# Optimization experiments

Measured on AMD Instinct MI355X. Metric: run time of the kernel, lower is better.

## Reference

```python
import jax, jax.numpy as jnp
import numpy as np

B = 4096
P_HID = 1024
H_HID = 512
MAX_P = 128
MAX_HE = MAX_P // 3  # 42
TAU = 1.0
EPS = 1e-20


def setup_inputs() -> dict:
    key = jax.random.key(0)
    ks = jax.random.split(key, 12)
    s_p = 1.0 / np.sqrt(P_HID)
    s_h = 1.0 / np.sqrt(H_HID)
    # gumbel noise: g = -log(-log(U))
    u_p = jax.random.uniform(ks[3], (B, MAX_P, 2), minval=EPS, maxval=1.0)
    u_h = jax.random.uniform(ks[4], (B, MAX_HE, 2), minval=EPS, maxval=1.0)
    return {
        "particle_h": jax.random.normal(ks[0], (B, P_HID), jnp.float32),
        "edge_h": jax.random.normal(ks[1], (B, H_HID), jnp.float32),
        "hyperedge_h": jax.random.normal(ks[2], (B, H_HID), jnp.float32),
        "g_p": -jnp.log(-jnp.log(u_p)),
        "g_h": -jnp.log(-jnp.log(u_h)),
        "W1_p": jax.random.normal(ks[5], (P_HID, P_HID), jnp.float32) * s_p,
        "b1_p": jnp.zeros((P_HID,), jnp.float32),
        "W2_p": jax.random.normal(ks[6], (P_HID, MAX_P), jnp.float32) * s_p,
        "b2_p": jnp.zeros((MAX_P,), jnp.float32),
        "W1_h": jax.random.normal(ks[7], (H_HID, H_HID), jnp.float32) * s_h,
        "b1_h": jnp.zeros((H_HID,), jnp.float32),
        "W2_h": jax.random.normal(ks[8], (H_HID, MAX_HE), jnp.float32) * s_h,
        "b2_h": jnp.zeros((MAX_HE,), jnp.float32),
    }


def _gumbel_hard_st(logits, g, tau):
    """F.gumbel_softmax(stack([l,-l],-1), tau, hard=True)[...,0] (straight-through)."""
    y = jax.nn.softmax((jnp.stack([logits, -logits], axis=-1) + g) / tau, axis=-1)
    y0 = y[..., 0]
    hard0 = (y0 > y[..., 1]).astype(y0.dtype)
    return hard0 + y0 - jax.lax.stop_gradient(y0)


def _mlp(x, W1, b1, W2, b2):
    return jax.nn.gelu(x @ W1 + b1, approximate=False) @ W2 + b2


def reference(particle_h, edge_h, hyperedge_h, g_p, g_h,
              W1_p, b1_p, W2_p, b2_p, W1_h, b1_h, W2_h, b2_h):
    particle_logits = _mlp(particle_h, W1_p, b1_p, W2_p, b2_p)      # [B, MAX_P]
    particle_mask = _gumbel_hard_st(particle_logits, g_p, TAU)      # [B, MAX_P]
    n_particles = particle_mask.sum(axis=-1).astype(jnp.int32)      # [B]

    # Ragged edge lists as a fixed padded buffer: all C(MAX_P,2) lexicographic
    # pairs (same order as torch.combinations); pair (i,j), i<j, is valid for
    # batch b iff j < n_particles[b].
    ii, jj = jnp.triu_indices(MAX_P, k=1)
    edge_index = jnp.stack([ii, jj]).astype(jnp.int32)              # [2, E_max]
    edge_valid = jj[None, :] < n_particles[:, None]                 # [B, E_max] bool

    hyperedge_logits = _mlp(hyperedge_h, W1_h, b1_h, W2_h, b2_h)    # [B, MAX_HE]
    hyperedge_mask = _gumbel_hard_st(hyperedge_logits, g_h, TAU)
    n_hyperedges = hyperedge_mask.sum(axis=-1).astype(jnp.int32)

    return (particle_mask, n_particles, edge_index, edge_valid,
            hyperedge_mask, n_hyperedges)
```

## Files before the change

### kernel.cpp

```cpp
#include <hip/hip_runtime.h>
#include <hip/hip_bf16.h>
#include <math.h>

typedef __bf16 bf16_t;
typedef bf16_t bf16x8 __attribute__((ext_vector_type(8)));
typedef bf16_t bf16x4 __attribute__((ext_vector_type(4)));
typedef float f32x4 __attribute__((ext_vector_type(4)));
typedef unsigned int u32;

#define B_SZ 4096
#define P_HID 1024
#define H_HID 512
#define MAX_P 128
#define MAX_HE 42
#define HE_PAD 128
#define E_MAX 8128
#define E_MAX4 2032

__device__ __forceinline__ void async_cp16(const bf16_t* g, bf16_t* l) {
    __builtin_amdgcn_global_load_lds(
        (const __attribute__((address_space(1))) u32*)g,
        (__attribute__((address_space(3))) u32*)l, 16, 0, 0);
}

__device__ __forceinline__ float gelu_exact(float v) {
    return 0.5f * v * (1.f + erff(v * 0.70710678118654752f));
}

struct GemmP {
    const bf16_t *Ahi, *Alo, *BThi, *BTlo;
    const float* bias;
    bf16_t *Chi, *Clo;
    const float* g;
    float *out_mask, *out_n;
    int *ws_n;
    int N, K, NV, nx;
};

template<int MODE>
__global__ __launch_bounds__(256, 4) void gemm_pack(GemmP P, GemmP H, int pBlocks)
{
    constexpr int BM = 64, BN = 128;
    constexpr int MT = 2, NT = 4;
    constexpr int OPS_A = BM / 16;
    constexpr int OPS_B = BN / 16;
    constexpr int NOPS = 2 * OPS_A + 2 * OPS_B;

    __shared__ __align__(16) bf16_t smem[(2 * BM + 2 * BN) * 32];
    __shared__ float cnt[BM][2];
    bf16_t* const As0 = smem;
    bf16_t* const As1 = smem + BM * 32;
    bf16_t* const Bs0 = smem + 2 * BM * 32;
    bf16_t* const Bs1 = smem + 2 * BM * 32 + BN * 32;

    const bool isP = (int)blockIdx.x < pBlocks;
    const GemmP& a = isP ? P : H;
    const int bid  = isP ? blockIdx.x : blockIdx.x - pBlocks;
    const int bn   = (bid % a.nx) * BN;
    const int bm   = (bid / a.nx) * BM;
    const int K    = a.K;

    const int tid  = threadIdx.x;
    const int lane = tid & 63;
    const int wid  = tid >> 6;
    const int wm   = wid & 1;
    const int wn   = wid >> 1;

    const int srow = lane >> 2;
    const int scol = (lane & 3) * 8;
    const int fr   = lane & 15;
    const int fq   = lane >> 4;

    f32x4 acc[MT][NT];
#pragma unroll
    for (int i = 0; i < MT; ++i)
#pragma unroll
        for (int j = 0; j < NT; ++j)
            acc[i][j] = (f32x4){0.f, 0.f, 0.f, 0.f};

    const bf16_t* const gA0 = a.Ahi  + (size_t)bm * K;
    const bf16_t* const gA1 = a.Alo  + (size_t)bm * K;
    const bf16_t* const gB0 = a.BThi + (size_t)bn * K;
    const bf16_t* const gB1 = a.BTlo + (size_t)bn * K;

    for (int kt = 0; kt < K; kt += 32) {
        __syncthreads();
#pragma unroll
        for (int o = 0; o < NOPS; ++o) {
            if ((o & 3) != wid) continue;
            const bf16_t* gsrc;
            bf16_t* lbase;
            int q;
            if (o < OPS_A)                  { q = o;                     gsrc = gA0; lbase = As0; }
            else if (o < 2 * OPS_A)         { q = o - OPS_A;             gsrc = gA1; lbase = As1; }
            else if (o < 2 * OPS_A + OPS_B) { q = o - 2 * OPS_A;         gsrc = gB0; lbase = Bs0; }
            else                            { q = o - 2 * OPS_A - OPS_B; gsrc = gB1; lbase = Bs1; }
            async_cp16(gsrc + (size_t)(q * 16 + srow) * K + kt + scol,
                       lbase + q * 16 * 32);
        }
        __syncthreads();

        bf16x8 ah[MT], al[MT], bh[NT], bl[NT];
#pragma unroll
        for (int i = 0; i < MT; ++i) {
            const int row = wm * 32 + i * 16 + fr;
            ah[i] = *(const bf16x8*)(As0 + row * 32 + fq * 8);
            al[i] = *(const bf16x8*)(As1 + row * 32 + fq * 8);
        }
#pragma unroll
        for (int j = 0; j < NT; ++j) {
            const int row = wn * 64 + j * 16 + fr;
            bh[j] = *(const bf16x8*)(Bs0 + row * 32 + fq * 8);
            bl[j] = *(const bf16x8*)(Bs1 + row * 32 + fq * 8);
        }
#pragma unroll
        for (int i = 0; i < MT; ++i)
#pragma unroll
            for (int j = 0; j < NT; ++j) {
                acc[i][j] = __builtin_amdgcn_mfma_f32_16x16x32_bf16(ah[i], bh[j], acc[i][j], 0, 0, 0);
                acc[i][j] = __builtin_amdgcn_mfma_f32_16x16x32_bf16(ah[i], bl[j], acc[i][j], 0, 0, 0);
                acc[i][j] = __builtin_amdgcn_mfma_f32_16x16x32_bf16(al[i], bh[j], acc[i][j], 0, 0, 0);
            }
    }

    if (MODE == 0) {
#pragma unroll
        for (int i = 0; i < MT; ++i)
#pragma unroll
            for (int j = 0; j < NT; ++j) {
                const int col  = bn + wn * 64 + j * 16 + fr;
                const int row0 = bm + wm * 32 + i * 16 + fq * 4;
                const float bj = a.bias[col];
#pragma unroll
                for (int r = 0; r < 4; ++r) {
                    float v = gelu_exact(acc[i][j][r] + bj);
                    bf16_t h = (bf16_t)v;
                    bf16_t l = (bf16_t)(v - (float)h);
                    const size_t off = (size_t)(row0 + r) * a.N + col;
                    a.Chi[off] = h;
                    a.Clo[off] = l;
                }
            }
    } else {
        const int NV = a.NV;
#pragma unroll
        for (int i = 0; i < MT; ++i) {
#pragma unroll
            for (int r = 0; r < 4; ++r) {
                const int row_l = wm * 32 + i * 16 + fq * 4 + r;
                const int grow  = bm + row_l;
                float s = 0.f;
#pragma unroll
                for (int j = 0; j < NT; ++j) {
                    const int col = wn * 64 + j * 16 + fr;
                    if (col < NV) {
                        const float v = acc[i][j][r] + a.bias[col];
                        const size_t idx = (size_t)grow * NV + col;
                        const float g0 = a.g[2 * idx + 0];
                        const float g1 = a.g[2 * idx + 1];
                        const float m = ((v + g0) > (g1 - v)) ? 1.f : 0.f;
                        a.out_mask[idx] = m;
                        s += m;
                    }
                }
                s += __shfl_xor(s, 1, 64);
                s += __shfl_xor(s, 2, 64);
                s += __shfl_xor(s, 4, 64);
                s += __shfl_xor(s, 8, 64);
                if (fr == 0) cnt[row_l][wn] = s;
            }
        }
        __syncthreads();
        if (tid < BM) {
            const float c = cnt[tid][0] + cnt[tid][1];
            a.out_n[bm + tid] = c;
            if (a.ws_n) a.ws_n[bm + tid] = (int)c;
        }
    }
}

struct PrepArgs {
    const float *ph, *hh, *W1p, *W2p, *W1h, *W2h;
    bf16_t *pA_hi, *pA_lo, *hA_hi, *hA_lo;
    bf16_t *W1pT_hi, *W1pT_lo, *W2pT_hi, *W2pT_lo;
    bf16_t *W1hT_hi, *W1hT_lo, *W2hT_hi, *W2hT_lo;
    float *out_ei; int *ws_jj;
};

__device__ __forceinline__ void split4(const float* x, bf16_t* hi, bf16_t* lo, int i) {
    float4 v = ((const float4*)x)[i];
    float vv[4] = {v.x, v.y, v.z, v.w};
    bf16x4 h, l;
#pragma unroll
    for (int r = 0; r < 4; ++r) {
        bf16_t hh = (bf16_t)vv[r];
        h[r] = hh;
        l[r] = (bf16_t)(vv[r] - (float)hh);
    }
    ((bf16x4*)hi)[i] = h;
    ((bf16x4*)lo)[i] = l;
}

__device__ __forceinline__ void tsplit(
    const float* W, bf16_t* Thi, bf16_t* Tlo, int K, int N,
    int t, int nx, float (*sh)[33], int tid)
{
    const int n0 = (t % nx) * 32, k0 = (t / nx) * 32;
    const int tx = tid & 31, ty = tid >> 5;
    for (int r = ty; r < 32; r += 8) {
        const int n = n0 + tx;
        sh[r][tx] = (n < N) ? W[(size_t)(k0 + r) * N + n] : 0.f;
    }
    __syncthreads();
    for (int r = ty; r < 32; r += 8) {
        const float x = sh[tx][r];
        bf16_t h = (bf16_t)x;
        bf16_t l = (bf16_t)(x - (float)h);
        const size_t off = (size_t)(n0 + r) * K + k0 + tx;
        Thi[off] = h;
        Tlo[off] = l;
    }
}

__device__ __forceinline__ int tri_off(int i) { return (i * (255 - i)) >> 1; }

__global__ __launch_bounds__(256) void prep_all(PrepArgs a)
{
    __shared__ float sh[32][33];
    const int bid = blockIdx.x;
    const int tid = threadIdx.x;

    if (bid < 4096) {
        split4(a.ph, a.pA_hi, a.pA_lo, bid * 256 + tid);
    } else if (bid < 6144) {
        split4(a.hh, a.hA_hi, a.hA_lo, (bid - 4096) * 256 + tid);
    } else if (bid < 7168) {
        tsplit(a.W1p, a.W1pT_hi, a.W1pT_lo, P_HID, P_HID, bid - 6144, 32, sh, tid);
    } else if (bid < 7296) {
        tsplit(a.W2p, a.W2pT_hi, a.W2pT_lo, P_HID, MAX_P, bid - 7168, 4, sh, tid);
    } else if (bid < 7552) {
        tsplit(a.W1h, a.W1hT_hi, a.W1hT_lo, H_HID, H_HID, bid - 7296, 16, sh, tid);
    } else if (bid < 7616) {
        tsplit(a.W2h, a.W2hT_hi, a.W2hT_lo, H_HID, MAX_HE, bid - 7552, 4, sh, tid);
    } else {
        const int e = (bid - 7616) * 256 + tid;
        if (e < E_MAX) {
            int i = (int)((255.0 - sqrt(65025.0 - 8.0 * (double)e)) * 0.5);
            if (i < 0) i = 0;
            if (i > 126) i = 126;
            while (i > 0 && tri_off(i) > e) --i;
            while (i < 126 && tri_off(i + 1) <= e) ++i;
            const int j = i + 1 + (e - tri_off(i));
            a.out_ei[e] = (float)i;
            a.out_ei[E_MAX + e] = (float)j;
            a.ws_jj[e] = j;
        }
    }
}

__global__ __launch_bounds__(256) void edge_valid_kernel(
    const int* __restrict__ ws_jj, const int* __restrict__ ws_n,
    float* __restrict__ out)
{
    const int b   = blockIdx.x >> 1;
    const int seg = blockIdx.x & 1;
    const int n   = ws_n[b];
    const int base = seg * (E_MAX4 / 2);
    float* const orow = out + (size_t)b * E_MAX;
#pragma unroll
    for (int it = 0; it < 4; ++it) {
        const int q = base + it * 256 + threadIdx.x;
        if (q < base + E_MAX4 / 2) {
            const int4 j4 = ((const int4*)ws_jj)[q];
            float4 v;
            v.x = (j4.x < n) ? 1.f : 0.f;
            v.y = (j4.y < n) ? 1.f : 0.f;
            v.z = (j4.z < n) ? 1.f : 0.f;
            v.w = (j4.w < n) ? 1.f : 0.f;
            ((float4*)orow)[q] = v;
        }
    }
}

extern "C" void kernel_launch(void* const* d_in, const int* in_sizes, int n_in,
                              void* d_out, int out_size, void* d_ws, size_t ws_size,
                              hipStream_t stream)
{
    const float* particle_h  = (const float*)d_in[0];
    const float* hyperedge_h = (const float*)d_in[2];
    const float* g_p  = (const float*)d_in[3];
    const float* g_h  = (const float*)d_in[4];
    const float* W1_p = (const float*)d_in[5];
    const float* b1_p = (const float*)d_in[6];
    const float* W2_p = (const float*)d_in[7];
    const float* b2_p = (const float*)d_in[8];
    const float* W1_h = (const float*)d_in[9];
    const float* b1_h = (const float*)d_in[10];
    const float* W2_h = (const float*)d_in[11];
    const float* b2_h = (const float*)d_in[12];

    float* out = (float*)d_out;
    float* out_pmask = out;
    float* out_np    = out_pmask + (size_t)B_SZ * MAX_P;
    float* out_ei    = out_np + B_SZ;
    float* out_ev    = out_ei + 2 * E_MAX;
    float* out_hmask = out_ev + (size_t)B_SZ * E_MAX;
    float* out_nh    = out_hmask + (size_t)B_SZ * MAX_HE;

    char* w = (char*)d_ws;
    bf16_t* pA_hi   = (bf16_t*)w;  w += (size_t)B_SZ * P_HID * 2;
    bf16_t* pA_lo   = (bf16_t*)w;  w += (size_t)B_SZ * P_HID * 2;
    bf16_t* hA_hi   = (bf16_t*)w;  w += (size_t)B_SZ * H_HID * 2;
    bf16_t* hA_lo   = (bf16_t*)w;  w += (size_t)B_SZ * H_HID * 2;
    bf16_t* hidp_hi = (bf16_t*)w;  w += (size_t)B_SZ * P_HID * 2;
    bf16_t* hidp_lo = (bf16_t*)w;  w += (size_t)B_SZ * P_HID * 2;
    bf16_t* hidh_hi = (bf16_t*)w;  w += (size_t)B_SZ * H_HID * 2;
    bf16_t* hidh_lo = (bf16_t*)w;  w += (size_t)B_SZ * H_HID * 2;
    bf16_t* W1pT_hi = (bf16_t*)w;  w += (size_t)P_HID * P_HID * 2;
    bf16_t* W1pT_lo = (bf16_t*)w;  w += (size_t)P_HID * P_HID * 2;
    bf16_t* W2pT_hi = (bf16_t*)w;  w += (size_t)MAX_P * P_HID * 2;
    bf16_t* W2pT_lo = (bf16_t*)w;  w += (size_t)MAX_P * P_HID * 2;
    bf16_t* W1hT_hi = (bf16_t*)w;  w += (size_t)H_HID * H_HID * 2;
    bf16_t* W1hT_lo = (bf16_t*)w;  w += (size_t)H_HID * H_HID * 2;
    bf16_t* W2hT_hi = (bf16_t*)w;  w += (size_t)HE_PAD * H_HID * 2;
    bf16_t* W2hT_lo = (bf16_t*)w;  w += (size_t)HE_PAD * H_HID * 2;
    int*    ws_np   = (int*)w;     w += B_SZ * 4;
    int*    ws_jj   = (int*)w;

    PrepArgs pa;
    pa.ph = particle_h; pa.hh = hyperedge_h;
    pa.W1p = W1_p; pa.W2p = W2_p; pa.W1h = W1_h; pa.W2h = W2_h;
    pa.pA_hi = pA_hi; pa.pA_lo = pA_lo; pa.hA_hi = hA_hi; pa.hA_lo = hA_lo;
    pa.W1pT_hi = W1pT_hi; pa.W1pT_lo = W1pT_lo;
    pa.W2pT_hi = W2pT_hi; pa.W2pT_lo = W2pT_lo;
    pa.W1hT_hi = W1hT_hi; pa.W1hT_lo = W1hT_lo;
    pa.W2hT_hi = W2hT_hi; pa.W2hT_lo = W2hT_lo;
    pa.out_ei = out_ei; pa.ws_jj = ws_jj;
    prep_all<<<7648, 256, 0, stream>>>(pa);

    {
        GemmP P = {}, H = {};
        P.Ahi = pA_hi;  P.Alo = pA_lo;  P.BThi = W1pT_hi; P.BTlo = W1pT_lo;
        P.bias = b1_p;  P.Chi = hidp_hi; P.Clo = hidp_lo;
        P.N = P_HID; P.K = P_HID; P.nx = P_HID / 128;
        H.Ahi = hA_hi;  H.Alo = hA_lo;  H.BThi = W1hT_hi; H.BTlo = W1hT_lo;
        H.bias = b1_h;  H.Chi = hidh_hi; H.Clo = hidh_lo;
        H.N = H_HID; H.K = H_HID; H.nx = H_HID / 128;
        const int pB = (B_SZ / 64) * P.nx;
        const int hB = (B_SZ / 64) * H.nx;
        gemm_pack<0><<<pB + hB, 256, 0, stream>>>(P, H, pB);
    }

    {
        GemmP P = {}, H = {};
        P.Ahi = hidp_hi; P.Alo = hidp_lo; P.BThi = W2pT_hi; P.BTlo = W2pT_lo;
        P.bias = b2_p; P.g = g_p; P.out_mask = out_pmask; P.out_n = out_np;
        P.ws_n = ws_np; P.N = MAX_P; P.K = P_HID; P.NV = MAX_P; P.nx = 1;
        H.Ahi = hidh_hi; H.Alo = hidh_lo; H.BThi = W2hT_hi; H.BTlo = W2hT_lo;
        H.bias = b2_h; H.g = g_h; H.out_mask = out_hmask; H.out_n = out_nh;
        H.ws_n = nullptr; H.N = HE_PAD; H.K = H_HID; H.NV = MAX_HE; H.nx = 1;
        const int pB = B_SZ / 64;
        const int hB = B_SZ / 64;
        gemm_pack<1><<<pB + hB, 256, 0, stream>>>(P, H, pB);
    }

    edge_valid_kernel<<<2 * B_SZ, 256, 0, stream>>>(ws_jj, ws_np, out_ev);
}
```

Before: 292.1 us.

## Split K across warp pairs in GEMM with shared-memory reduction

The GEMM kernel now loads a 64-wide K slice per iteration and gives each pair of warps its own 32-wide half, so each warp covers the full M tile. The two partial accumulators are then summed through shared memory before the epilogue. This halves the number of barrier-separated K iterations. The second GEMM uses BM=32, which doubles its block count for better occupancy. The change also lowers launch bounds to 3 blocks per CU, uses more LDS, adds a reduction step, and switches edge_valid stores to nontemporal.

```diff
diff --git a/kernel.cpp b/kernel.cpp
--- a/kernel.cpp
+++ b/kernel.cpp
@@ -6,6 +6,7 @@
 typedef bf16_t bf16x8 __attribute__((ext_vector_type(8)));
 typedef bf16_t bf16x4 __attribute__((ext_vector_type(4)));
 typedef float f32x4 __attribute__((ext_vector_type(4)));
+typedef int i32x4 __attribute__((ext_vector_type(4)));
 typedef unsigned int u32;
 
 #define B_SZ 4096
@@ -37,21 +38,19 @@
     int N, K, NV, nx;
 };
 
-template<int MODE>
-__global__ __launch_bounds__(256, 4) void gemm_pack(GemmP P, GemmP H, int pBlocks)
-{
-    constexpr int BM = 64, BN = 128;
-    constexpr int MT = 2, NT = 4;
+template<int MODE, int BM>
+__global__ __launch_bounds__(256, 3) void gemm_pack(GemmP P, GemmP H, int pBlocks)
+{
+    constexpr int BN = 128;
+    constexpr int MT = BM / 16;
+    constexpr int NT = 4;
     constexpr int OPS_A = BM / 16;
     constexpr int OPS_B = BN / 16;
     constexpr int NOPS = 2 * OPS_A + 2 * OPS_B;
-
-    __shared__ __align__(16) bf16_t smem[(2 * BM + 2 * BN) * 32];
+    constexpr int TILE = NOPS * 16 * 32;
+
+    __shared__ __align__(16) bf16_t smem[2 * TILE];
     __shared__ float cnt[BM][2];
-    bf16_t* const As0 = smem;
-    bf16_t* const As1 = smem + BM * 32;
-    bf16_t* const Bs0 = smem + 2 * BM * 32;
-    bf16_t* const Bs1 = smem + 2 * BM * 32 + BN * 32;
 
     const bool isP = (int)blockIdx.x < pBlocks;
     const GemmP& a = isP ? P : H;
@@ -63,8 +62,8 @@
     const int tid  = threadIdx.x;
     const int lane = tid & 63;
     const int wid  = tid >> 6;
-    const int wm   = wid & 1;
-    const int wn   = wid >> 1;
+    const int wn   = wid & 1;
+    const int pair = wid >> 1;
 
     const int srow = lane >> 2;
     const int scol = (lane & 3) * 8;
@@ -83,93 +82,120 @@
     const bf16_t* const gB0 = a.BThi + (size_t)bn * K;
     const bf16_t* const gB1 = a.BTlo + (size_t)bn * K;
 
-    for (int kt = 0; kt < K; kt += 32) {
+    bf16_t* const Tme = smem + pair * TILE;
+
+    for (int kt = 0; kt < K; kt += 64) {
         __syncthreads();
 #pragma unroll
-        for (int o = 0; o < NOPS; ++o) {
+        for (int o = 0; o < 2 * NOPS; ++o) {
             if ((o & 3) != wid) continue;
+            const int half = (o < NOPS) ? 0 : 1;
+            const int oo   = o - half * NOPS;
             const bf16_t* gsrc;
-            bf16_t* lbase;
-            int q;
-            if (o < OPS_A)                  { q = o;                     gsrc = gA0; lbase = As0; }
-            else if (o < 2 * OPS_A)         { q = o - OPS_A;             gsrc = gA1; lbase = As1; }
-            else if (o < 2 * OPS_A + OPS_B) { q = o - 2 * OPS_A;         gsrc = gB0; lbase = Bs0; }
-            else                            { q = o - 2 * OPS_A - OPS_B; gsrc = gB1; lbase = Bs1; }
-            async_cp16(gsrc + (size_t)(q * 16 + srow) * K + kt + scol,
-                       lbase + q * 16 * 32);
+            int q, sec;
+            if (oo < OPS_A)                  { q = oo;                     gsrc = gA0; sec = 0; }
+            else if (oo < 2 * OPS_A)         { q = oo - OPS_A;             gsrc = gA1; sec = BM * 32; }
+            else if (oo < 2 * OPS_A + OPS_B) { q = oo - 2 * OPS_A;         gsrc = gB0; sec = 2 * BM * 32; }
+            else                             { q = oo - 2 * OPS_A - OPS_B; gsrc = gB1; sec = 2 * BM * 32 + BN * 32; }
+            async_cp16(gsrc + (size_t)(q * 16 + srow) * K + kt + half * 32 + scol,
+                       smem + half * TILE + sec + q * 16 * 32);
         }
         __syncthreads();
 
-        bf16x8 ah[MT], al[MT], bh[NT], bl[NT];
+        bf16x8 ah[MT], al[MT];
 #pragma unroll
         for (int i = 0; i < MT; ++i) {
-            const int row = wm * 32 + i * 16 + fr;
-            ah[i] = *(const bf16x8*)(As0 + row * 32 + fq * 8);
-            al[i] = *(const bf16x8*)(As1 + row * 32 + fq * 8);
+            const int row = i * 16 + fr;
+            ah[i] = *(const bf16x8*)(Tme + row * 32 + fq * 8);
+            al[i] = *(const bf16x8*)(Tme + BM * 32 + row * 32 + fq * 8);
         }
 #pragma unroll
         for (int j = 0; j < NT; ++j) {
             const int row = wn * 64 + j * 16 + fr;
-            bh[j] = *(const bf16x8*)(Bs0 + row * 32 + fq * 8);
-            bl[j] = *(const bf16x8*)(Bs1 + row * 32 + fq * 8);
-        }
+            const bf16x8 bh = *(const bf16x8*)(Tme + 2 * BM * 32 + row * 32 + fq * 8);
+            const bf16x8 bl = *(const bf16x8*)(Tme + 2 * BM * 32 + BN * 32 + row * 32 + fq * 8);
+#pragma unroll
+            for (int i = 0; i < MT; ++i) {
+                acc[i][j] = __builtin_amdgcn_mfma_f32_16x16x32_bf16(ah[i], bh, acc[i][j], 0, 0, 0);
+                acc[i][j] = __builtin_amdgcn_mfma_f32_16x16x32_bf16(ah[i], bl, acc[i][j], 0, 0, 0);
+                acc[i][j] = __builtin_amdgcn_mfma_f32_16x16x32_bf16(al[i], bh, acc[i][j], 0, 0, 0);
+            }
+        }
+    }
+
+    float* const cb = (float*)smem;
+    __syncthreads();
+    if (pair == 1) {
 #pragma unroll
         for (int i = 0; i < MT; ++i)
 #pragma unroll
-            for (int j = 0; j < NT; ++j) {
-                acc[i][j] = __builtin_amdgcn_mfma_f32_16x16x32_bf16(ah[i], bh[j], acc[i][j], 0, 0, 0);
-                acc[i][j] = __builtin_amdgcn_mfma_f32_16x16x32_bf16(ah[i], bl[j], acc[i][j], 0, 0, 0);
-                acc[i][j] = __builtin_amdgcn_mfma_f32_16x16x32_bf16(al[i], bh[j], acc[i][j], 0, 0, 0);
-            }
-    }
-
-    if (MODE == 0) {
+            for (int j = 0; j < NT; ++j)
+#pragma unroll
+                for (int r = 0; r < 4; ++r)
+                    cb[(i * 16 + fq * 4 + r) * BN + wn * 64 + j * 16 + fr] = acc[i][j][r];
+    }
+    __syncthreads();
+
+    if (pair == 0) {
 #pragma unroll
         for (int i = 0; i < MT; ++i)
 #pragma unroll
-            for (int j = 0; j < NT; ++j) {
-                const int col  = bn + wn * 64 + j * 16 + fr;
-                const int row0 = bm + wm * 32 + i * 16 + fq * 4;
-                const float bj = a.bias[col];
+            for (int j = 0; j < NT; ++j)
+#pragma unroll
+                for (int r = 0; r < 4; ++r)
+                    acc[i][j][r] += cb[(i * 16 + fq * 4 + r) * BN + wn * 64 + j * 16 + fr];
+
+        if (MODE == 0) {
+#pragma unroll
+            for (int i = 0; i < MT; ++i)
+#pragma unroll
+                for (int j = 0; j < NT; ++j) {
+                    const int col  = bn + wn * 64 + j * 16 + fr;
+                    const int row0 = bm + i * 16 + fq * 4;
+                    const float bj = a.bias[col];
+#pragma unroll
+                    for (int r = 0; r < 4; ++r) {
+                        float v = gelu_exact(acc[i][j][r] + bj);
+                        bf16_t h = (bf16_t)v;
+                        bf16_t l = (bf16_t)(v - (float)h);
+                        const size_t off = (size_t)(row0 + r) * a.N + col;
+                        a.Chi[off] = h;
+                        a.Clo[off] = l;
+                    }
+                }
+        } else {
+            const int NV = a.NV;
+#pragma unroll
+            for (int i = 0; i < MT; ++i) {
 #pragma unroll
                 for (int r = 0; r < 4; ++r) {
-                    float v = gelu_exact(acc[i][j][r] + bj);
-                    bf16_t h = (bf16_t)v;
-                    bf16_t l = (bf16_t)(v - (float)h);
-                    const size_t off = (size_t)(row0 + r) * a.N + col;
-                    a.Chi[off] = h;
-                    a.Clo[off] = l;
+                    const int row_l = i * 16 + fq * 4 + r;
+                    const int grow  = bm + row_l;
+                    float s = 0.f;
+#pragma unroll
+                    for (int j = 0; j < NT; ++j) {
+                        const int col = wn * 64 + j * 16 + fr;
+                        if (col < NV) {
+                            const float v = acc[i][j][r] + a.bias[col];
+                            const size_t idx = (size_t)grow * NV + col;
+                            const float g0 = a.g[2 * idx + 0];
+                            const float g1 = a.g[2 * idx + 1];
+                            const float m = ((v + g0) > (g1 - v)) ? 1.f : 0.f;
+                            a.out_mask[idx] = m;
+                            s += m;
+                        }
+                    }
+                    s += __shfl_xor(s, 1, 64);
+                    s += __shfl_xor(s, 2, 64);
+                    s += __shfl_xor(s, 4, 64);
+                    s += __shfl_xor(s, 8, 64);
+                    if (fr == 0) cnt[row_l][wn] = s;
                 }
             }
-    } else {
-        const int NV = a.NV;
-#pragma unroll
-        for (int i = 0; i < MT; ++i) {
-#pragma unroll
-            for (int r = 0; r < 4; ++r) {
-                const int row_l = wm * 32 + i * 16 + fq * 4 + r;
-                const int grow  = bm + row_l;
-                float s = 0.f;
-#pragma unroll
-                for (int j = 0; j < NT; ++j) {
-                    const int col = wn * 64 + j * 16 + fr;
-                    if (col < NV) {
-                        const float v = acc[i][j][r] + a.bias[col];
-                        const size_t idx = (size_t)grow * NV + col;
-                        const float g0 = a.g[2 * idx + 0];
-                        const float g1 = a.g[2 * idx + 1];
-                        const float m = ((v + g0) > (g1 - v)) ? 1.f : 0.f;
-                        a.out_mask[idx] = m;
-                        s += m;
-                    }
-                }
-                s += __shfl_xor(s, 1, 64);
-                s += __shfl_xor(s, 2, 64);
-                s += __shfl_xor(s, 4, 64);
-                s += __shfl_xor(s, 8, 64);
-                if (fr == 0) cnt[row_l][wn] = s;
-            }
-        }
+        }
+    }
+
+    if (MODE == 1) {
         __syncthreads();
         if (tid < BM) {
             const float c = cnt[tid][0] + cnt[tid][1];
@@ -271,13 +297,13 @@
     for (int it = 0; it < 4; ++it) {
         const int q = base + it * 256 + threadIdx.x;
         if (q < base + E_MAX4 / 2) {
-            const int4 j4 = ((const int4*)ws_jj)[q];
-            float4 v;
+            const i32x4 j4 = ((const i32x4*)ws_jj)[q];
+            f32x4 v;
             v.x = (j4.x < n) ? 1.f : 0.f;
             v.y = (j4.y < n) ? 1.f : 0.f;
             v.z = (j4.z < n) ? 1.f : 0.f;
             v.w = (j4.w < n) ? 1.f : 0.f;
-            ((float4*)orow)[q] = v;
+            __builtin_nontemporal_store(v, &((f32x4*)orow)[q]);
         }
     }
 }
@@ -348,7 +374,7 @@
         H.N = H_HID; H.K = H_HID; H.nx = H_HID / 128;
         const int pB = (B_SZ / 64) * P.nx;
         const int hB = (B_SZ / 64) * H.nx;
-        gemm_pack<0><<<pB + hB, 256, 0, stream>>>(P, H, pB);
+        gemm_pack<0, 64><<<pB + hB, 256, 0, stream>>>(P, H, pB);
     }
 
     {
@@ -359,9 +385,9 @@
         H.Ahi = hidh_hi; H.Alo = hidh_lo; H.BThi = W2hT_hi; H.BTlo = W2hT_lo;
         H.bias = b2_h; H.g = g_h; H.out_mask = out_hmask; H.out_n = out_nh;
         H.ws_n = nullptr; H.N = HE_PAD; H.K = H_HID; H.NV = MAX_HE; H.nx = 1;
-        const int pB = B_SZ / 64;
-        const int hB = B_SZ / 64;
-        gemm_pack<1><<<pB + hB, 256, 0, stream>>>(P, H, pB);
+        const int pB = B_SZ / 32;
+        const int hB = B_SZ / 32;
+        gemm_pack<1, 32><<<pB + hB, 256, 0, stream>>>(P, H, pB);
     }
 
     edge_valid_kernel<<<2 * B_SZ, 256, 0, stream>>>(ws_jj, ws_np, out_ev);
```

Result: no change. 287.1 us (-1.7%).
